# Kernel optimization log

Hardware: AMD Instinct MI355X
Metric: run time of the kernel (lower is better)

## Reference

```python
import jax, jax.numpy as jnp
import numpy as np

EPS = 1e-3  # Keras BatchNormalization default epsilon
K = 7

def _bn(x, gamma, beta, mean, var):
    return gamma * (x - mean) * jax.lax.rsqrt(var + EPS) + beta

def setup_inputs() -> dict:
    key = jax.random.key(0)
    ks = jax.random.split(key, 4)
    B, L, Cin, F = 64, 512, 64, 128
    out_len = L - K + 1
    return {
        "x": jax.random.normal(ks[0], (B, L, Cin), jnp.float32),
        "conv_w": jax.random.normal(ks[1], (K, Cin, F), jnp.float32) * (1.0 / np.sqrt(K * Cin)),
        "conv_b": jnp.zeros((F,), jnp.float32),
        "bn1_gamma": jnp.ones((F,), jnp.float32),
        "bn1_beta": jnp.zeros((F,), jnp.float32),
        "bn1_mean": jnp.zeros((F,), jnp.float32),
        "bn1_var": jnp.ones((F,), jnp.float32),
        "local_w": jax.random.normal(ks[2], (out_len, K * F, F), jnp.float32) * (1.0 / np.sqrt(K * F)),
        "local_b": jnp.zeros((out_len, F), jnp.float32),
        "bn2_gamma": jnp.ones((F,), jnp.float32),
        "bn2_beta": jnp.zeros((F,), jnp.float32),
        "bn2_mean": jnp.zeros((F,), jnp.float32),
        "bn2_var": jnp.ones((F,), jnp.float32),
    }

def reference(x, conv_w, conv_b, bn1_gamma, bn1_beta, bn1_mean, bn1_var,
              local_w, local_b, bn2_gamma, bn2_beta, bn2_mean, bn2_var):
    # Conv1D, padding='same'  (NWC / WIO)
    y = jax.lax.conv_general_dilated(
        x, conv_w, window_strides=(1,), padding="SAME",
        dimension_numbers=("NWC", "WIO", "NWC")) + conv_b
    y = jax.nn.relu(_bn(y, bn1_gamma, bn1_beta, bn1_mean, bn1_var))

    # LocallyConnected1D, padding='valid': per-position unshared weights
    B, L, F = y.shape
    out_len = L - K + 1
    idx = jnp.arange(out_len)[:, None] + jnp.arange(K)[None, :]  # (out_len, K)
    patches = y[:, idx, :].reshape(B, out_len, K * F)             # (B, out_len, K*F)
    z = jnp.einsum("blk,lkf->blf", patches, local_w) + local_b    # (B, out_len, F)
    z = jax.nn.relu(_bn(z, bn2_gamma, bn2_beta, bn2_mean, bn2_var))
    return z
```

## Files before the change

### kernel.cpp

```cpp
#include <hip/hip_runtime.h>
#include <hip/hip_bf16.h>

typedef __attribute__((ext_vector_type(8))) short bf16x8;
typedef __attribute__((ext_vector_type(4))) float f32x4;

#define BB   64
#define LL   512
#define CIN  64
#define FF   128
#define KW   7
#define OUTL 506
#define LPAD 518
#define KC   448
#define KL   896
#define BK2  64
#define NCH2 14
#define EPSV 1e-3f

#define NPAD  (BB * LPAD * CIN)
#define PADB  (NPAD / 256)
#define NWT   (FF * KC)
#define WTB   (NWT / 256)

static __device__ __forceinline__ short f2bf(float f) {
    unsigned u = __builtin_bit_cast(unsigned, f);
    unsigned r = (u + 0x7fffu + ((u >> 16) & 1u)) >> 16;
    return (short)r;
}

static __device__ __forceinline__ void g2lds16(const float* g, float* l) {
    __builtin_amdgcn_global_load_lds(
        (const __attribute__((address_space(1))) unsigned int*)g,
        (__attribute__((address_space(3))) unsigned int*)l, 16, 0, 0);
}

__global__ void prep_kernel(const float* __restrict__ x, const float* __restrict__ w,
                            short* __restrict__ xp, short* __restrict__ wt) {
    if (blockIdx.x < PADB) {
        int i = blockIdx.x * 256 + threadIdx.x;
        int c  = i & (CIN - 1);
        int t  = i >> 6;
        int lp = t % LPAD;
        int b  = t / LPAD;
        float v = 0.0f;
        int l = lp - 3;
        if (l >= 0 && l < LL) v = x[(b * LL + l) * CIN + c];
        xp[i] = f2bf(v);
    } else {
        int i = (blockIdx.x - PADB) * 256 + threadIdx.x;
        int n = i / KC;
        int k = i - n * KC;
        wt[i] = f2bf(w[(size_t)k * FF + n]);
    }
}

__global__ __launch_bounds__(256) void conv_bn_kernel(
    const short* __restrict__ xp, const short* __restrict__ wt,
    const float* __restrict__ cb, const float* __restrict__ g,
    const float* __restrict__ be, const float* __restrict__ mu,
    const float* __restrict__ va, short* __restrict__ y) {
    const int lane = threadIdx.x & 63;
    const int wid  = threadIdx.x >> 6;
    const int m0   = blockIdx.x * 64;
    const int nb   = wid * 32;
    const int q    = lane >> 4;
    const int ln   = lane & 15;

    const short* arow[4];
#pragma unroll
    for (int mt = 0; mt < 4; ++mt) {
        int m = m0 + mt * 16 + ln;
        int b = m >> 9, l = m & 511;
        arow[mt] = xp + (b * LPAD + l) * CIN;
    }
    const short* brow[2];
#pragma unroll
    for (int nt = 0; nt < 2; ++nt)
        brow[nt] = wt + (size_t)(nb + nt * 16 + ln) * KC;

    f32x4 acc[4][2];
#pragma unroll
    for (int mt = 0; mt < 4; ++mt)
#pragma unroll
        for (int nt = 0; nt < 2; ++nt) acc[mt][nt] = (f32x4){0.f, 0.f, 0.f, 0.f};

#pragma unroll 2
    for (int kc = 0; kc < KC; kc += 32) {
        const int ko = kc + q * 8;
        bf16x8 a[4], bf[2];
#pragma unroll
        for (int mt = 0; mt < 4; ++mt) a[mt] = *(const bf16x8*)(arow[mt] + ko);
#pragma unroll
        for (int nt = 0; nt < 2; ++nt) bf[nt] = *(const bf16x8*)(brow[nt] + ko);
#pragma unroll
        for (int mt = 0; mt < 4; ++mt)
#pragma unroll
            for (int nt = 0; nt < 2; ++nt)
                acc[mt][nt] = __builtin_amdgcn_mfma_f32_16x16x32_bf16(
                    a[mt], bf[nt], acc[mt][nt], 0, 0, 0);
    }

#pragma unroll
    for (int nt = 0; nt < 2; ++nt) {
        const int n = nb + nt * 16 + ln;
        const float s  = g[n] * rsqrtf(va[n] + EPSV);
        const float b2 = s * (cb[n] - mu[n]) + be[n];
#pragma unroll
        for (int mt = 0; mt < 4; ++mt) {
            const int mbase = m0 + mt * 16 + q * 4;
#pragma unroll
            for (int r = 0; r < 4; ++r) {
                float v = fmaxf(acc[mt][nt][r] * s + b2, 0.0f);
                y[(size_t)(mbase + r) * FF + n] = f2bf(v);
            }
        }
    }
}

__global__ __launch_bounds__(256) void local_bn_kernel(
    const short* __restrict__ y, const float* __restrict__ lw,
    const float* __restrict__ lb, const float* __restrict__ g,
    const float* __restrict__ be, const float* __restrict__ mu,
    const float* __restrict__ va, float* __restrict__ out) {
    __shared__ float wtile[2][BK2 * 64];
    const int l    = blockIdx.x >> 1;
    const int h    = blockIdx.x & 1;
    const int lane = threadIdx.x & 63;
    const int wid  = threadIdx.x >> 6;
    const int q    = lane >> 4;
    const int ln   = lane & 15;
    const int nl   = wid * 16 + ln;

    const float* wlh = lw + (size_t)l * (KL * FF) + h * 64;

    const short* arow[4];
#pragma unroll
    for (int mt = 0; mt < 4; ++mt)
        arow[mt] = y + (size_t)(mt * 16 + ln) * (LL * FF) + (size_t)l * FF;

    f32x4 acc[4];
#pragma unroll
    for (int mt = 0; mt < 4; ++mt) acc[mt] = (f32x4){0.f, 0.f, 0.f, 0.f};

#define STAGE(kc_, buf_)                                                        \
    {                                                                           \
        _Pragma("unroll")                                                       \
        for (int r = 0; r < 4; ++r) {                                           \
            const int ib   = (r * 4 + wid) * 256;                               \
            const int e    = ib + lane * 4;                                     \
            const int row  = e >> 6;                                            \
            const int colp = e & 63;                                            \
            const int col  = colp ^ (((row >> 3) & 1) << 4);                    \
            g2lds16(wlh + (size_t)((kc_) + row) * FF + col, &(buf_)[ib]);       \
        }                                                                       \
    }

    STAGE(0, wtile[0]);

    for (int c = 0; c < NCH2; ++c) {
        __syncthreads();
        if (c + 1 < NCH2) STAGE((c + 1) * BK2, wtile[(c + 1) & 1]);
        const float* wb = wtile[c & 1];

#pragma unroll
        for (int s = 0; s < 2; ++s) {
            const int ko = c * BK2 + s * 32 + q * 8;
            bf16x8 a[4];
#pragma unroll
            for (int mt = 0; mt < 4; ++mt) a[mt] = *(const bf16x8*)(arow[mt] + ko);

            bf16x8 bfr;
#pragma unroll
            for (int j = 0; j < 8; ++j) {
                const int row = s * 32 + q * 8 + j;
                const int col = nl ^ (((row >> 3) & 1) << 4);
                bfr[j] = f2bf(wb[row * 64 + col]);
            }
#pragma unroll
            for (int mt = 0; mt < 4; ++mt)
                acc[mt] = __builtin_amdgcn_mfma_f32_16x16x32_bf16(
                    a[mt], bfr, acc[mt], 0, 0, 0);
        }
    }
#undef STAGE

    const int n = h * 64 + nl;
    const float s  = g[n] * rsqrtf(va[n] + EPSV);
    const float b2 = s * (lb[(size_t)l * FF + n] - mu[n]) + be[n];
#pragma unroll
    for (int mt = 0; mt < 4; ++mt) {
        const int bbase = mt * 16 + q * 4;
#pragma unroll
        for (int r = 0; r < 4; ++r) {
            float v = fmaxf(acc[mt][r] * s + b2, 0.0f);
            out[(size_t)(bbase + r) * (OUTL * FF) + (size_t)l * FF + n] = v;
        }
    }
}

extern "C" void kernel_launch(void* const* d_in, const int* in_sizes, int n_in,
                              void* d_out, int out_size, void* d_ws, size_t ws_size,
                              hipStream_t stream) {
    const float* x       = (const float*)d_in[0];
    const float* conv_w  = (const float*)d_in[1];
    const float* conv_b  = (const float*)d_in[2];
    const float* bn1_g   = (const float*)d_in[3];
    const float* bn1_b   = (const float*)d_in[4];
    const float* bn1_m   = (const float*)d_in[5];
    const float* bn1_v   = (const float*)d_in[6];
    const float* local_w = (const float*)d_in[7];
    const float* local_b = (const float*)d_in[8];
    const float* bn2_g   = (const float*)d_in[9];
    const float* bn2_b   = (const float*)d_in[10];
    const float* bn2_m   = (const float*)d_in[11];
    const float* bn2_v   = (const float*)d_in[12];
    float* out = (float*)d_out;

    short* xp  = (short*)d_ws;
    short* ybf = xp + (size_t)NPAD;
    short* wt  = ybf + (size_t)BB * LL * FF;

    prep_kernel<<<PADB + WTB, 256, 0, stream>>>(x, conv_w, xp, wt);
    conv_bn_kernel<<<(BB * LL) / 64, 256, 0, stream>>>(
        xp, wt, conv_b, bn1_g, bn1_b, bn1_m, bn1_v, ybf);
    local_bn_kernel<<<2 * OUTL, 256, 0, stream>>>(
        ybf, local_w, local_b, bn2_g, bn2_b, bn2_m, bn2_v, out);
}
```

Measured before the change: 380.2 us.

## Triple-buffer local weight staging and prefetch local weights into cache during conv

The local-connected kernel moves from a double-buffered to a triple-buffered LDS pipeline. It keeps two chunks in flight and waits with explicit vmcnt counts and a raw barrier instead of __syncthreads. Separately, the conv kernel launches extra blocks that read the first 32KB of each position's local weights, so those bytes are warm in the cache when the second kernel starts. The trade is more LDS use per block, which can lower occupancy, extra read traffic during the conv phase, and reliance on a fragile hand-set waitcnt.

```diff
diff --git a/kernel.cpp b/kernel.cpp
--- a/kernel.cpp
+++ b/kernel.cpp
@@ -21,6 +21,10 @@
 #define PADB  (NPAD / 256)
 #define NWT   (FF * KC)
 #define WTB   (NWT / 256)
+
+#define CONVB ((BB * LL) / 64)
+#define WARMB OUTL
+#define WARMV 2048
 
 static __device__ __forceinline__ short f2bf(float f) {
     unsigned u = __builtin_bit_cast(unsigned, f);
@@ -58,7 +62,20 @@
     const short* __restrict__ xp, const short* __restrict__ wt,
     const float* __restrict__ cb, const float* __restrict__ g,
     const float* __restrict__ be, const float* __restrict__ mu,
-    const float* __restrict__ va, short* __restrict__ y) {
+    const float* __restrict__ va, short* __restrict__ y,
+    const float* __restrict__ lw) {
+    if (blockIdx.x >= CONVB) {
+        const int wb = blockIdx.x - CONVB;
+        const f32x4* src = (const f32x4*)(lw + (size_t)wb * (KL * FF));
+        float s = 0.f;
+        for (int i = threadIdx.x; i < WARMV; i += 256) {
+            f32x4 v = src[i];
+            s += v[0] + v[1] + v[2] + v[3];
+        }
+        asm volatile("" :: "v"(s));
+        return;
+    }
+
     const int lane = threadIdx.x & 63;
     const int wid  = threadIdx.x >> 6;
     const int m0   = blockIdx.x * 64;
@@ -122,7 +139,7 @@
     const float* __restrict__ lb, const float* __restrict__ g,
     const float* __restrict__ be, const float* __restrict__ mu,
     const float* __restrict__ va, float* __restrict__ out) {
-    __shared__ float wtile[2][BK2 * 64];
+    __shared__ float wtile[3][BK2 * 64];
     const int l    = blockIdx.x >> 1;
     const int h    = blockIdx.x & 1;
     const int lane = threadIdx.x & 63;
@@ -156,11 +173,20 @@
     }
 
     STAGE(0, wtile[0]);
+    STAGE(BK2, wtile[1]);
 
     for (int c = 0; c < NCH2; ++c) {
-        __syncthreads();
-        if (c + 1 < NCH2) STAGE((c + 1) * BK2, wtile[(c + 1) & 1]);
-        const float* wb = wtile[c & 1];
+        if (c < NCH2 - 1) {
+            asm volatile("s_waitcnt vmcnt(4)" ::: "memory");
+        } else {
+            asm volatile("s_waitcnt vmcnt(0)" ::: "memory");
+        }
+        __builtin_amdgcn_s_barrier();
+        __builtin_amdgcn_sched_barrier(0);
+
+        if (c + 2 < NCH2) STAGE((c + 2) * BK2, wtile[(c + 2) % 3]);
+
+        const float* wb = wtile[c % 3];
 
 #pragma unroll
         for (int s = 0; s < 2; ++s) {
@@ -221,8 +247,8 @@
     short* wt  = ybf + (size_t)BB * LL * FF;
 
     prep_kernel<<<PADB + WTB, 256, 0, stream>>>(x, conv_w, xp, wt);
-    conv_bn_kernel<<<(BB * LL) / 64, 256, 0, stream>>>(
-        xp, wt, conv_b, bn1_g, bn1_b, bn1_m, bn1_v, ybf);
+    conv_bn_kernel<<<CONVB + WARMB, 256, 0, stream>>>(
+        xp, wt, conv_b, bn1_g, bn1_b, bn1_m, bn1_v, ybf, local_w);
     local_bn_kernel<<<2 * OUTL, 256, 0, stream>>>(
         ybf, local_w, local_b, bn2_g, bn2_b, bn2_m, bn2_v, out);
 }
```

Result: no change. 383.9 us (+1.0%).
